# Optimization experiments

Hardware: AMD Instinct MI355X
Metric: run time of the kernel (lower is better)

## Reference

```python
import math
import jax, jax.numpy as jnp
from jax import lax
import numpy as np

B, S2, D = 8, 1024, 768  # seq_len = 32*32 spatial tokens
HD = 64                   # head_dim
K = 7                     # LocalRmsNorm kernel_size
EPS = 1e-7


def setup_inputs() -> dict:
    key = jax.random.key(0)
    ks = jax.random.split(key, 6)
    sc = 0.02
    return {
        "x": jax.random.normal(ks[0], (B, S2, D), jnp.float32),
        "norm_w": jnp.ones((D,), jnp.float32),
        "wq": jax.random.normal(ks[1], (D, D), jnp.float32) * sc,
        "bq": jnp.zeros((D,), jnp.float32),
        "wk": jax.random.normal(ks[2], (D, D), jnp.float32) * sc,
        "bk": jnp.zeros((D,), jnp.float32),
        "wv": jax.random.normal(ks[3], (D, D), jnp.float32) * sc,
        "bv": jnp.zeros((D,), jnp.float32),
        "wo": jax.random.normal(ks[4], (D, D), jnp.float32) * sc,
        "bo": jnp.zeros((D,), jnp.float32),
    }


def local_rms_norm(x, w):
    # x: [b, s*s, d]; sliding KxK box-sum of squares over the s x s grid,
    # zero-padded (matches F.unfold), mean divisor is always K*K.
    b, ss, d = x.shape
    s = int(math.isqrt(ss))
    sq = (x * x).reshape(b, s, s, d)
    box = lax.reduce_window(sq, 0.0, lax.add,
                            (1, K, K, 1), (1, 1, 1, 1), 'SAME')
    rms = jnp.sqrt(EPS + box / (K * K)).reshape(b, ss, d)
    return x / rms * w


def reference(x, norm_w, wq, bq, wk, bk, wv, bv, wo, bo):
    xn = local_rms_norm(x, norm_w)
    b, s, d = xn.shape
    h = d // HD

    def proj(w_, b_):
        return (xn @ w_.T + b_).reshape(b, s, h, HD).transpose(0, 2, 1, 3)

    q = proj(wq, bq)  # [b, h, s, dh]
    k = proj(wk, bk)
    v = proj(wv, bv)
    scores = jnp.einsum('bhqd,bhkd->bhqk', q, k) / math.sqrt(HD)
    attn = jax.nn.softmax(scores, axis=-1)
    out = jnp.einsum('bhqk,bhkd->bhqd', attn, v)
    out = out.transpose(0, 2, 1, 3).reshape(b, s, d)
    return out @ wo.T + bo
```

## Files before the change

### kernel.cpp

```cpp
#include <hip/hip_runtime.h>

typedef _Float16 f16x8 __attribute__((ext_vector_type(8)));
typedef _Float16 f16x4 __attribute__((ext_vector_type(4)));
typedef _Float16 f16x2 __attribute__((ext_vector_type(2)));
typedef float    f32x4 __attribute__((ext_vector_type(4)));
typedef float    f32x16 __attribute__((ext_vector_type(16)));
typedef unsigned int u32x4 __attribute__((ext_vector_type(4)));
typedef unsigned short ushort_t;
typedef unsigned int uint_t;

#define LOG2E 1.44269504088896340736f

#define CFENCE  asm volatile("" ::: "memory")
#define HWBAR   __builtin_amdgcn_s_barrier()
#define VMCNT0  asm volatile("s_waitcnt vmcnt(0)" ::: "memory")
#define VMCNT3  asm volatile("s_waitcnt vmcnt(3)" ::: "memory")
#define VMCNT4  asm volatile("s_waitcnt vmcnt(4)" ::: "memory")

__device__ __forceinline__ ushort_t f2h(float x) {
  _Float16 h = (_Float16)x;
  return __builtin_bit_cast(ushort_t, h);
}

__device__ __forceinline__ uint_t packpair(float a, float b) {
  return __builtin_bit_cast(uint_t, __builtin_amdgcn_cvt_pkrtz(a, b));
}

__device__ __forceinline__ f16x8 mk8(uint_t a, uint_t b, uint_t c, uint_t d) {
  u32x4 t; t[0] = a; t[1] = b; t[2] = c; t[3] = d;
  return __builtin_bit_cast(f16x8, t);
}

__device__ __forceinline__ void gload_lds16(const void* g, void* lds) {
  __builtin_amdgcn_global_load_lds(
      (const __attribute__((address_space(1))) void*)(uintptr_t)g,
      (__attribute__((address_space(3))) void*)(unsigned)(uintptr_t)lds,
      16, 0, 0);
}


__global__ __launch_bounds__(256)
void lrn_a(const float* __restrict__ x, ushort_t* __restrict__ tmp) {
  int tid = blockIdx.x * 256 + threadIdx.x;
  int dv  = tid % 192;
  int rem = tid / 192;
  int pos = rem & 1023;
  int b   = rem >> 10;
  int r = pos >> 5, c = pos & 31;
  const float4* base = (const float4*)x + ((size_t)b * 1024 + (size_t)r * 32) * 192 + dv;
  float ax = 0.f, ay = 0.f, az = 0.f, aw = 0.f;
#pragma unroll
  for (int dc = -3; dc <= 3; ++dc) {
    int cc = c + dc;
    if (cc >= 0 && cc < 32) {
      float4 v = base[cc * 192];
      ax += v.x * v.x; ay += v.y * v.y; az += v.z * v.z; aw += v.w * v.w;
    }
  }
  f16x4 o;
  o[0] = (_Float16)ax; o[1] = (_Float16)ay; o[2] = (_Float16)az; o[3] = (_Float16)aw;
  *(f16x4*)(tmp + (size_t)tid * 4) = o;
}

__global__ __launch_bounds__(256)
void lrn_b(const float* __restrict__ x, const ushort_t* __restrict__ tmp,
           const float* __restrict__ wn, ushort_t* __restrict__ xn) {
  int tid = blockIdx.x * 256 + threadIdx.x;
  int dv  = tid % 192;
  int rem = tid / 192;
  int pos = rem & 1023;
  int b   = rem >> 10;
  int r = pos >> 5, c = pos & 31;
  const ushort_t* tb = tmp + (((size_t)b * 1024 + c) * 192 + dv) * 4;
  float ax = 0.f, ay = 0.f, az = 0.f, aw = 0.f;
#pragma unroll
  for (int dr = -3; dr <= 3; ++dr) {
    int rr = r + dr;
    if (rr >= 0 && rr < 32) {
      f16x4 v = *(const f16x4*)(tb + (size_t)rr * 24576);
      ax += (float)v[0]; ay += (float)v[1]; az += (float)v[2]; aw += (float)v[3];
    }
  }
  float4 xv = ((const float4*)x)[tid];
  float4 wv = ((const float4*)wn)[dv];
  const float inv49 = 1.0f / 49.0f;
  float i0 = 1.0f / sqrtf(1e-7f + ax * inv49);
  float i1 = 1.0f / sqrtf(1e-7f + ay * inv49);
  float i2 = 1.0f / sqrtf(1e-7f + az * inv49);
  float i3 = 1.0f / sqrtf(1e-7f + aw * inv49);
  f16x4 o;
  o[0] = (_Float16)(xv.x * i0 * wv.x);
  o[1] = (_Float16)(xv.y * i1 * wv.y);
  o[2] = (_Float16)(xv.z * i2 * wv.z);
  o[3] = (_Float16)(xv.w * i3 * wv.w);
  const int m = b * 1024 + pos;
  const int panel = m >> 4, lrr = m & 15;
  const int kc = dv >> 3, lg2 = (dv >> 1) & 3, half = dv & 1;
  *(f16x4*)(xn + ((size_t)((panel * 24 + kc) * 64 + lg2 * 16 + lrr)) * 8 + half * 4) = o;
}

__global__ __launch_bounds__(256)
void convw_fm(const float* __restrict__ wq, const float* __restrict__ wk,
              const float* __restrict__ wv, const float* __restrict__ wo,
              ushort_t* __restrict__ bqkv, ushort_t* __restrict__ bwo) {
  const int g = blockIdx.x * 256 + threadIdx.x;
  const int mat = g / 73728;
  const int gg = g % 73728;
  const int panel = gg / 1536;
  const int rem = gg % 1536;
  const int kc = rem >> 6, l = rem & 63;
  const int row = panel * 16 + (l & 15);
  const int col = kc * 32 + (l >> 4) * 8;
  const float* src = (mat == 0) ? wq : (mat == 1) ? wk : (mat == 2) ? wv : wo;
  const float4 v0 = *(const float4*)(src + (size_t)row * 768 + col);
  const float4 v1 = *(const float4*)(src + (size_t)row * 768 + col + 4);
  f16x8 o;
  o[0]=(_Float16)v0.x; o[1]=(_Float16)v0.y; o[2]=(_Float16)v0.z; o[3]=(_Float16)v0.w;
  o[4]=(_Float16)v1.x; o[5]=(_Float16)v1.y; o[6]=(_Float16)v1.z; o[7]=(_Float16)v1.w;
  if (mat < 3) *(f16x8*)(bqkv + (size_t)g * 8) = o;
  else         *(f16x8*)(bwo  + (size_t)gg * 8) = o;
}

#define GSTAGE(BUF, KT) do {                                                      \
    _Pragma("unroll")                                                             \
    for (int j = 0; j < SI; ++j)                                                  \
      gload_lds16(sb[j] + (KT) * 512, (BUF) ? d1[j] : d0[j]);                     \
  } while (0)

#define GTILE(KT, CUR, NXT) do {                                                  \
    CFENCE; HWBAR; CFENCE;                              \
    if ((KT) + 1 < 24) {                                                          \
      GSTAGE(NXT, (KT) + 1);                                                      \
      if constexpr (SI == 4) VMCNT4; else VMCNT3;       \
    } else VMCNT0;                                                                \
    CFENCE; HWBAR;                                \
    __builtin_amdgcn_sched_barrier(0);                                            \
    f16x8 af[MT], bf[NT];                                                         \
    _Pragma("unroll")                                                             \
    for (int mt = 0; mt < MT; ++mt)                                               \
      af[mt] = *(const f16x8*)(&As[CUR][(wr * MT + mt) * 512 + l * 8]);           \
    _Pragma("unroll")                                                             \
    for (int nt = 0; nt < NT; ++nt)                                               \
      bf[nt] = *(const f16x8*)(&Bs[CUR][(wc * NT + nt) * 512 + l * 8]);           \
    _Pragma("unroll")                                                             \
    for (int mt = 0; mt < MT; ++mt)                                               \
      _Pragma("unroll")                                                           \
      for (int nt = 0; nt < NT; ++nt)                                             \
        acc[mt][nt] = __builtin_amdgcn_mfma_f32_16x16x32_f16(af[mt], bf[nt], acc[mt][nt], 0, 0, 0); \
  } while (0)

template <int MODE>
__global__ __launch_bounds__(256)
void gemm_lds(const ushort_t* __restrict__ Afm, const ushort_t* __restrict__ Bfm,
              const float* __restrict__ b0, const float* __restrict__ b1,
              const float* __restrict__ b2,
              ushort_t* __restrict__ q, ushort_t* __restrict__ k,
              ushort_t* __restrict__ v, float* __restrict__ outf) {
  constexpr int PM  = (MODE == 0) ? 8 : 4;
  constexpr int PN  = 8;
  constexpr int NBN = (MODE == 0) ? 18 : 6;
  constexpr int SI  = (PM + PN) / 4;
  constexpr int MT  = PM / 2, NT = PN / 2;
  __shared__ __align__(16) ushort_t As[2][PM * 512];
  __shared__ __align__(16) ushort_t Bs[2][PN * 512];

  const int nwg = gridDim.x;
  const int bid = blockIdx.x;
  const int cid = (bid & 7) * (nwg >> 3) + (bid >> 3);
  const int bm = cid / NBN, bn = cid % NBN;
  const int tid = threadIdx.x;
  const int w = tid >> 6, l = tid & 63;
  const int wr = w >> 1, wc = w & 1;
  const int lr = l & 15, lg = l >> 4;

  f32x4 acc[MT][NT] = {};

  const ushort_t* sb[SI];
  ushort_t* d0[SI];
  ushort_t* d1[SI];
#pragma unroll
  for (int j = 0; j < SI; ++j) {
    const int g = w * SI + j;
    if (g < PM) {
      sb[j] = Afm + ((size_t)(bm * PM + g) * 24) * 512 + l * 8;
      d0[j] = &As[0][g * 512]; d1[j] = &As[1][g * 512];
    } else {
      sb[j] = Bfm + ((size_t)(bn * PN + (g - PM)) * 24) * 512 + l * 8;
      d0[j] = &Bs[0][(g - PM) * 512]; d1[j] = &Bs[1][(g - PM) * 512];
    }
  }

  GSTAGE(0, 0);
  for (int kt = 0; kt < 24; kt += 2) {
    GTILE(kt, 0, 1);
    GTILE(kt + 1, 1, 0);
  }

#pragma unroll
  for (int mt = 0; mt < MT; ++mt) {
#pragma unroll
    for (int nt = 0; nt < NT; ++nt) {
      if (MODE == 0) {
        const int n = bn * 128 + wc * 64 + nt * 16 + lr;
        const int mbase = bm * 128 + wr * 64 + mt * 16 + lg * 4;
        const int region = n / 768;
        const int nn = n - region * 768;
        const int hh = nn >> 6, hd = nn & 63;
        const float bb = (region == 0 ? b0 : region == 1 ? b1 : b2)[nn];
        if (region == 2) {
          const int bi = mbase >> 10, s0 = mbase & 1023;
          const int tile = s0 >> 6, q6 = s0 & 63;
          const int aa = q6 >> 5, r5 = q6 & 31;
          const int t1 = r5 >> 3, h2 = (r5 >> 2) & 1;
          const int gq = t1 >> 1, jj = (2 * t1) & 3;
          const int s0p = (tile << 6) + (((aa << 1) + gq) << 4) + (h2 << 3) + 2 * jj;
          f16x4 pv;
#pragma unroll
          for (int gi = 0; gi < 4; ++gi) pv[gi] = (_Float16)(acc[mt][nt][gi] + bb);
          *(f16x4*)(v + (((size_t)(bi * 12 + hh)) * 64 + hd) * 1024 + s0p) = pv;
        } else {
#pragma unroll
          for (int gi = 0; gi < 4; ++gi) {
            const int m = mbase + gi;
            const int bi = m >> 10, s = m & 1023;
            const float val = acc[mt][nt][gi] + bb;
            if (region == 0)
              q[(((size_t)(bi * 12 + hh)) * 1024 + s) * 64 + hd] = f2h(val * (0.125f * LOG2E));
            else
              k[(((size_t)(bi * 12 + hh)) * 1024 + s) * 64 + hd] = f2h(val);
          }
        }
      } else {
        const int n = bn * 128 + wc * 64 + nt * 16 + lr;
        const float bb = b0[n];
#pragma unroll
        for (int gi = 0; gi < 4; ++gi) {
          const int m = bm * 64 + wr * 32 + mt * 16 + lg * 4 + gi;
          outf[(size_t)m * 768 + n] = acc[mt][nt][gi] + bb;
        }
      }
    }
  }
}

#define ATILE(T, CUR, NXT) do {                                                   \
    CFENCE; HWBAR; CFENCE;                              \
    if ((T) < 15) {                                                               \
      const int kv0n = ((T) + 1) << 6;                                            \
      gload_lds16(kp + (size_t)(kv0n + r1) * 64 + s1 * 8,  Kl0 + (NXT) * 8192);   \
      gload_lds16(kp + (size_t)(kv0n + r2) * 64 + s2 * 8,  Kl1 + (NXT) * 8192);   \
      gload_lds16(vp + (size_t)r1 * 1024 + kv0n + s1 * 8,  Vl0 + (NXT) * 8192);   \
      gload_lds16(vp + (size_t)r2 * 1024 + kv0n + s2 * 8,  Vl1 + (NXT) * 8192);   \
      VMCNT4;                                        \
    } else VMCNT0;                                                                \
    CFENCE; HWBAR;                            \
    __builtin_amdgcn_sched_barrier(0);                                            \
    const char* kbase = (const char*)smem + (CUR) * 8192;                         \
    const char* vbase = (const char*)smem + 16384 + (CUR) * 8192;                 \
    f16x8 ka0[4], ka1[4];                                                         \
    _Pragma("unroll")                                                             \
    for (int kc = 0; kc < 4; ++kc) {                                              \
      ka0[kc] = *(const f16x8*)(kbase + off[kc]);                                 \
      ka1[kc] = *(const f16x8*)(kbase + off[kc] + 4096);                          \
    }                                                                             \
    f32x16 s0v = {}, s1v = {};                                                    \
    __builtin_amdgcn_s_setprio(1);                                                \
    _Pragma("unroll")                                                             \
    for (int kc = 0; kc < 4; ++kc) {                                              \
      s0v = __builtin_amdgcn_mfma_f32_32x32x16_f16(ka0[kc], qf[kc], s0v, 0, 0, 0);\
      s1v = __builtin_amdgcn_mfma_f32_32x32x16_f16(ka1[kc], qf[kc], s1v, 0, 0, 0);\
    }                                                                             \
    __builtin_amdgcn_s_setprio(0);                                                \
    f16x8 va0[4], va1[4];                                                         \
    _Pragma("unroll")                                                             \
    for (int c = 0; c < 4; ++c) {                                                 \
      va0[c] = *(const f16x8*)(vbase + off[c]);                                   \
      va1[c] = *(const f16x8*)(vbase + off[c] + 4096);                            \
    }                                                                             \
    uint_t pk0[8], pk1[8];                                                        \
    _Pragma("unroll")                                                             \
    for (int tt = 0; tt < 8; ++tt) {                                              \
      pk0[tt] = packpair(__builtin_exp2f(s0v[2 * tt]), __builtin_exp2f(s0v[2 * tt + 1])); \
      pk1[tt] = packpair(__builtin_exp2f(s1v[2 * tt]), __builtin_exp2f(s1v[2 * tt + 1])); \
    }                                                                             \
    _Pragma("unroll")                                                             \
    for (int tt = 0; tt < 4; ++tt) {                                              \
      lr0 = __builtin_amdgcn_fdot2(__builtin_bit_cast(f16x2, pk0[tt]),     one2, lr0, false); \
      lr1 = __builtin_amdgcn_fdot2(__builtin_bit_cast(f16x2, pk0[tt + 4]), one2, lr1, false); \
      lr2 = __builtin_amdgcn_fdot2(__builtin_bit_cast(f16x2, pk1[tt]),     one2, lr2, false); \
      lr3 = __builtin_amdgcn_fdot2(__builtin_bit_cast(f16x2, pk1[tt + 4]), one2, lr3, false); \
    }                                                                             \
    const f16x8 pb0 = mk8(pk0[0], pk0[1], pk0[2], pk0[3]);                        \
    const f16x8 pb1 = mk8(pk0[4], pk0[5], pk0[6], pk0[7]);                        \
    const f16x8 pb2 = mk8(pk1[0], pk1[1], pk1[2], pk1[3]);                        \
    const f16x8 pb3 = mk8(pk1[4], pk1[5], pk1[6], pk1[7]);                        \
    __builtin_amdgcn_s_setprio(1);                                                \
    oacc0 = __builtin_amdgcn_mfma_f32_32x32x16_f16(va0[0], pb0, oacc0, 0, 0, 0);  \
    oacc1 = __builtin_amdgcn_mfma_f32_32x32x16_f16(va1[0], pb0, oacc1, 0, 0, 0);  \
    oacc0 = __builtin_amdgcn_mfma_f32_32x32x16_f16(va0[1], pb1, oacc0, 0, 0, 0);  \
    oacc1 = __builtin_amdgcn_mfma_f32_32x32x16_f16(va1[1], pb1, oacc1, 0, 0, 0);  \
    oacc0 = __builtin_amdgcn_mfma_f32_32x32x16_f16(va0[2], pb2, oacc0, 0, 0, 0);  \
    oacc1 = __builtin_amdgcn_mfma_f32_32x32x16_f16(va1[2], pb2, oacc1, 0, 0, 0);  \
    oacc0 = __builtin_amdgcn_mfma_f32_32x32x16_f16(va0[3], pb3, oacc0, 0, 0, 0);  \
    oacc1 = __builtin_amdgcn_mfma_f32_32x32x16_f16(va1[3], pb3, oacc1, 0, 0, 0);  \
    __builtin_amdgcn_s_setprio(0);                                                \
  } while (0)

__global__ __launch_bounds__(256, 3)
void attn_fused7(const ushort_t* __restrict__ qb, const ushort_t* __restrict__ kb,
                 const ushort_t* __restrict__ vt, ushort_t* __restrict__ ao) {
  __shared__ __align__(16) ushort_t smem[16384];
  const int tid = threadIdx.x;
  const int w = tid >> 6, l = tid & 63;
  const int lq = l & 31, hi = l >> 5;

  const int bid = blockIdx.x;
  const int cid = (bid & 7) * 96 + (bid >> 3);
  const int bh = cid >> 3, qt = cid & 7;
  const int b = bh / 12, h = bh % 12;

  const ushort_t* qp = qb + ((size_t)bh * 1024 + qt * 128 + w * 32) * 64;
  const ushort_t* kp = kb + (size_t)bh * 65536;
  const ushort_t* vp = vt + (size_t)bh * 65536;

  f16x8 qf[4];
#pragma unroll
  for (int kc = 0; kc < 4; ++kc)
    qf[kc] = *(const f16x8*)(qp + lq * 64 + kc * 16 + hi * 8);

  const int r1 = tid >> 3,          s1 = (tid & 7) ^ (r1 & 7);
  const int r2 = (tid + 256) >> 3,  s2 = (tid & 7) ^ (r2 & 7);
  char* Kl0 = (char*)smem + w * 1024;
  char* Kl1 = (char*)smem + 4096 + w * 1024;
  char* Vl0 = (char*)smem + 16384 + w * 1024;
  char* Vl1 = (char*)smem + 16384 + 4096 + w * 1024;

  const int cswz = lq & 7;
  int off[4];
#pragma unroll
  for (int kc = 0; kc < 4; ++kc)
    off[kc] = lq * 128 + (((kc * 2 + hi) ^ cswz) * 16);

  f32x16 oacc0 = {}, oacc1 = {};
  float lr0 = 0.f, lr1 = 0.f, lr2 = 0.f, lr3 = 0.f;
  const f16x2 one2 = {(_Float16)1.f, (_Float16)1.f};

  gload_lds16(kp + (size_t)r1 * 64 + s1 * 8,   Kl0);
  gload_lds16(kp + (size_t)r2 * 64 + s2 * 8,   Kl1);
  gload_lds16(vp + (size_t)r1 * 1024 + s1 * 8, Vl0);
  gload_lds16(vp + (size_t)r2 * 1024 + s2 * 8, Vl1);

  for (int t2 = 0; t2 < 16; t2 += 2) {
    ATILE(t2, 0, 1);
    ATILE(t2 + 1, 1, 0);
  }

  float lrun = (lr0 + lr1) + (lr2 + lr3);
  lrun += __shfl_xor(lrun, 32, 64);
  const float invl = 1.0f / lrun;

  __syncthreads();

  uint_t* ot = (uint_t*)smem + w * 1024 + lq * 32;
#pragma unroll
  for (int tt = 0; tt < 8; ++tt) {
    const int base = (tt & 1) + ((tt >> 1) << 2) + 2 * hi;
    ot[base ^ lq]        = packpair(oacc0[2 * tt] * invl, oacc0[2 * tt + 1] * invl);
    ot[(base + 16) ^ lq] = packpair(oacc1[2 * tt] * invl, oacc1[2 * tt + 1] * invl);
  }
  __syncthreads();
  const int row = tid >> 1, halfc = tid & 1;
  const int w2 = row >> 5, qq = row & 31;
  const uint_t* srcp = (const uint_t*)smem + w2 * 1024 + qq * 32;
  const int m = b * 1024 + qt * 128 + row;
  const int panel = m >> 4, lrr = m & 15;
  const int kc = h * 2 + halfc;
#pragma unroll
  for (int jj = 0; jj < 4; ++jj) {
    u32x4 tv;
#pragma unroll
    for (int i2 = 0; i2 < 4; ++i2)
      tv[i2] = srcp[(halfc * 16 + jj * 4 + i2) ^ qq];
    *(u32x4*)(ao + ((size_t)((panel * 24 + kc) * 64 + jj * 16 + lrr)) * 8) = tv;
  }
}

extern "C" void kernel_launch(void* const* d_in, const int* in_sizes, int n_in,
                              void* d_out, int out_size, void* d_ws, size_t ws_size,
                              hipStream_t stream) {
  const float* x  = (const float*)d_in[0];
  const float* nw = (const float*)d_in[1];
  const float* wq = (const float*)d_in[2];
  const float* bq = (const float*)d_in[3];
  const float* wk = (const float*)d_in[4];
  const float* bk = (const float*)d_in[5];
  const float* wv = (const float*)d_in[6];
  const float* bv = (const float*)d_in[7];
  const float* wo = (const float*)d_in[8];
  const float* bo = (const float*)d_in[9];
  float* out = (float*)d_out;

  char* ws = (char*)d_ws;
  ushort_t* tmp   = (ushort_t*)ws;
  ushort_t* qbuf  = (ushort_t*)(ws);
  ushort_t* kbuf  = (ushort_t*)(ws + 12582912);
  ushort_t* xnf   = (ushort_t*)(ws + 25165824);
  ushort_t* bwqkv = (ushort_t*)(ws + 37748736);
  ushort_t* bwo   = (ushort_t*)(ws + 41287680);
  ushort_t* vtb   = (ushort_t*)(ws + 42467328);
  ushort_t* aoutf = (ushort_t*)(ws + 55050240);

  lrn_a<<<6144, 256, 0, stream>>>(x, tmp);
  lrn_b<<<6144, 256, 0, stream>>>(x, tmp, nw, xnf);
  convw_fm<<<1152, 256, 0, stream>>>(wq, wk, wv, wo, bwqkv, bwo);
  gemm_lds<0><<<1152, 256, 0, stream>>>(xnf, bwqkv, bq, bk, bv,
                                        qbuf, kbuf, vtb, nullptr);
  attn_fused7<<<768, 256, 0, stream>>>(qbuf, kbuf, vtb, aoutf);
  gemm_lds<1><<<768, 256, 0, stream>>>(aoutf, bwo, bo, nullptr, nullptr,
                                       nullptr, nullptr, nullptr, out);
}
```

Baseline: 147.3 us.

## Triple-buffer LDS tiles in attention and output GEMM to drop a barrier

The attention kernel and the output-projection GEMM move from double- to triple-buffered LDS staging with a rotating buffer index. Because the buffer being refilled was last read two iterations earlier, the barrier that used to come before issuing the next prefetch is removed, leaving one workgroup barrier per tile. The aim is to cut synchronisation stalls and let global-to-LDS loads overlap compute further. In exchange, attention LDS per block grows from 32KB to 48KB, which may limit occupancy at 3 blocks per CU, and the templated GEMM is split into two specialised kernels.

```diff
diff --git a/kernel.cpp b/kernel.cpp
--- a/kernel.cpp
+++ b/kernel.cpp
@@ -131,7 +131,7 @@
     CFENCE; HWBAR; CFENCE;                              \
     if ((KT) + 1 < 24) {                                                          \
       GSTAGE(NXT, (KT) + 1);                                                      \
-      if constexpr (SI == 4) VMCNT4; else VMCNT3;       \
+      VMCNT4;                                           \
     } else VMCNT0;                                                                \
     CFENCE; HWBAR;                                \
     __builtin_amdgcn_sched_barrier(0);                                            \
@@ -149,18 +149,13 @@
         acc[mt][nt] = __builtin_amdgcn_mfma_f32_16x16x32_f16(af[mt], bf[nt], acc[mt][nt], 0, 0, 0); \
   } while (0)
 
-template <int MODE>
 __global__ __launch_bounds__(256)
-void gemm_lds(const ushort_t* __restrict__ Afm, const ushort_t* __restrict__ Bfm,
+void gemm_qkv(const ushort_t* __restrict__ Afm, const ushort_t* __restrict__ Bfm,
               const float* __restrict__ b0, const float* __restrict__ b1,
               const float* __restrict__ b2,
               ushort_t* __restrict__ q, ushort_t* __restrict__ k,
-              ushort_t* __restrict__ v, float* __restrict__ outf) {
-  constexpr int PM  = (MODE == 0) ? 8 : 4;
-  constexpr int PN  = 8;
-  constexpr int NBN = (MODE == 0) ? 18 : 6;
-  constexpr int SI  = (PM + PN) / 4;
-  constexpr int MT  = PM / 2, NT = PN / 2;
+              ushort_t* __restrict__ v) {
+  constexpr int PM = 8, PN = 8, NBN = 18, SI = 4, MT = 4, NT = 4;
   __shared__ __align__(16) ushort_t As[2][PM * 512];
   __shared__ __align__(16) ushort_t Bs[2][PN * 512];
 
@@ -200,116 +195,113 @@
   for (int mt = 0; mt < MT; ++mt) {
 #pragma unroll
     for (int nt = 0; nt < NT; ++nt) {
-      if (MODE == 0) {
-        const int n = bn * 128 + wc * 64 + nt * 16 + lr;
-        const int mbase = bm * 128 + wr * 64 + mt * 16 + lg * 4;
-        const int region = n / 768;
-        const int nn = n - region * 768;
-        const int hh = nn >> 6, hd = nn & 63;
-        const float bb = (region == 0 ? b0 : region == 1 ? b1 : b2)[nn];
-        if (region == 2) {
-          const int bi = mbase >> 10, s0 = mbase & 1023;
-          const int tile = s0 >> 6, q6 = s0 & 63;
-          const int aa = q6 >> 5, r5 = q6 & 31;
-          const int t1 = r5 >> 3, h2 = (r5 >> 2) & 1;
-          const int gq = t1 >> 1, jj = (2 * t1) & 3;
-          const int s0p = (tile << 6) + (((aa << 1) + gq) << 4) + (h2 << 3) + 2 * jj;
-          f16x4 pv;
-#pragma unroll
-          for (int gi = 0; gi < 4; ++gi) pv[gi] = (_Float16)(acc[mt][nt][gi] + bb);
-          *(f16x4*)(v + (((size_t)(bi * 12 + hh)) * 64 + hd) * 1024 + s0p) = pv;
-        } else {
-#pragma unroll
-          for (int gi = 0; gi < 4; ++gi) {
-            const int m = mbase + gi;
-            const int bi = m >> 10, s = m & 1023;
-            const float val = acc[mt][nt][gi] + bb;
-            if (region == 0)
-              q[(((size_t)(bi * 12 + hh)) * 1024 + s) * 64 + hd] = f2h(val * (0.125f * LOG2E));
-            else
-              k[(((size_t)(bi * 12 + hh)) * 1024 + s) * 64 + hd] = f2h(val);
-          }
-        }
+      const int n = bn * 128 + wc * 64 + nt * 16 + lr;
+      const int mbase = bm * 128 + wr * 64 + mt * 16 + lg * 4;
+      const int region = n / 768;
+      const int nn = n - region * 768;
+      const int hh = nn >> 6, hd = nn & 63;
+      const float bb = (region == 0 ? b0 : region == 1 ? b1 : b2)[nn];
+      if (region == 2) {
+        const int bi = mbase >> 10, s0 = mbase & 1023;
+        const int tile = s0 >> 6, q6 = s0 & 63;
+        const int aa = q6 >> 5, r5 = q6 & 31;
+        const int t1 = r5 >> 3, h2 = (r5 >> 2) & 1;
+        const int gq = t1 >> 1, jj = (2 * t1) & 3;
+        const int s0p = (tile << 6) + (((aa << 1) + gq) << 4) + (h2 << 3) + 2 * jj;
+        f16x4 pv;
+#pragma unroll
+        for (int gi = 0; gi < 4; ++gi) pv[gi] = (_Float16)(acc[mt][nt][gi] + bb);
+        *(f16x4*)(v + (((size_t)(bi * 12 + hh)) * 64 + hd) * 1024 + s0p) = pv;
       } else {
-        const int n = bn * 128 + wc * 64 + nt * 16 + lr;
-        const float bb = b0[n];
 #pragma unroll
         for (int gi = 0; gi < 4; ++gi) {
-          const int m = bm * 64 + wr * 32 + mt * 16 + lg * 4 + gi;
-          outf[(size_t)m * 768 + n] = acc[mt][nt][gi] + bb;
+          const int m = mbase + gi;
+          const int bi = m >> 10, s = m & 1023;
+          const float val = acc[mt][nt][gi] + bb;
+          if (region == 0)
+            q[(((size_t)(bi * 12 + hh)) * 1024 + s) * 64 + hd] = f2h(val * (0.125f * LOG2E));
+          else
+            k[(((size_t)(bi * 12 + hh)) * 1024 + s) * 64 + hd] = f2h(val);
         }
       }
     }
   }
 }
 
-#define ATILE(T, CUR, NXT) do {                                                   \
-    CFENCE; HWBAR; CFENCE;                              \
-    if ((T) < 15) {                                                               \
-      const int kv0n = ((T) + 1) << 6;                                            \
-      gload_lds16(kp + (size_t)(kv0n + r1) * 64 + s1 * 8,  Kl0 + (NXT) * 8192);   \
-      gload_lds16(kp + (size_t)(kv0n + r2) * 64 + s2 * 8,  Kl1 + (NXT) * 8192);   \
-      gload_lds16(vp + (size_t)r1 * 1024 + kv0n + s1 * 8,  Vl0 + (NXT) * 8192);   \
-      gload_lds16(vp + (size_t)r2 * 1024 + kv0n + s2 * 8,  Vl1 + (NXT) * 8192);   \
-      VMCNT4;                                        \
-    } else VMCNT0;                                                                \
-    CFENCE; HWBAR;                            \
-    __builtin_amdgcn_sched_barrier(0);                                            \
-    const char* kbase = (const char*)smem + (CUR) * 8192;                         \
-    const char* vbase = (const char*)smem + 16384 + (CUR) * 8192;                 \
-    f16x8 ka0[4], ka1[4];                                                         \
-    _Pragma("unroll")                                                             \
-    for (int kc = 0; kc < 4; ++kc) {                                              \
-      ka0[kc] = *(const f16x8*)(kbase + off[kc]);                                 \
-      ka1[kc] = *(const f16x8*)(kbase + off[kc] + 4096);                          \
-    }                                                                             \
-    f32x16 s0v = {}, s1v = {};                                                    \
-    __builtin_amdgcn_s_setprio(1);                                                \
-    _Pragma("unroll")                                                             \
-    for (int kc = 0; kc < 4; ++kc) {                                              \
-      s0v = __builtin_amdgcn_mfma_f32_32x32x16_f16(ka0[kc], qf[kc], s0v, 0, 0, 0);\
-      s1v = __builtin_amdgcn_mfma_f32_32x32x16_f16(ka1[kc], qf[kc], s1v, 0, 0, 0);\
-    }                                                                             \
-    __builtin_amdgcn_s_setprio(0);                                                \
-    f16x8 va0[4], va1[4];                                                         \
-    _Pragma("unroll")                                                             \
-    for (int c = 0; c < 4; ++c) {                                                 \
-      va0[c] = *(const f16x8*)(vbase + off[c]);                                   \
-      va1[c] = *(const f16x8*)(vbase + off[c] + 4096);                            \
-    }                                                                             \
-    uint_t pk0[8], pk1[8];                                                        \
-    _Pragma("unroll")                                                             \
-    for (int tt = 0; tt < 8; ++tt) {                                              \
-      pk0[tt] = packpair(__builtin_exp2f(s0v[2 * tt]), __builtin_exp2f(s0v[2 * tt + 1])); \
-      pk1[tt] = packpair(__builtin_exp2f(s1v[2 * tt]), __builtin_exp2f(s1v[2 * tt + 1])); \
-    }                                                                             \
-    _Pragma("unroll")                                                             \
-    for (int tt = 0; tt < 4; ++tt) {                                              \
-      lr0 = __builtin_amdgcn_fdot2(__builtin_bit_cast(f16x2, pk0[tt]),     one2, lr0, false); \
-      lr1 = __builtin_amdgcn_fdot2(__builtin_bit_cast(f16x2, pk0[tt + 4]), one2, lr1, false); \
-      lr2 = __builtin_amdgcn_fdot2(__builtin_bit_cast(f16x2, pk1[tt]),     one2, lr2, false); \
-      lr3 = __builtin_amdgcn_fdot2(__builtin_bit_cast(f16x2, pk1[tt + 4]), one2, lr3, false); \
-    }                                                                             \
-    const f16x8 pb0 = mk8(pk0[0], pk0[1], pk0[2], pk0[3]);                        \
-    const f16x8 pb1 = mk8(pk0[4], pk0[5], pk0[6], pk0[7]);                        \
-    const f16x8 pb2 = mk8(pk1[0], pk1[1], pk1[2], pk1[3]);                        \
-    const f16x8 pb3 = mk8(pk1[4], pk1[5], pk1[6], pk1[7]);                        \
-    __builtin_amdgcn_s_setprio(1);                                                \
-    oacc0 = __builtin_amdgcn_mfma_f32_32x32x16_f16(va0[0], pb0, oacc0, 0, 0, 0);  \
-    oacc1 = __builtin_amdgcn_mfma_f32_32x32x16_f16(va1[0], pb0, oacc1, 0, 0, 0);  \
-    oacc0 = __builtin_amdgcn_mfma_f32_32x32x16_f16(va0[1], pb1, oacc0, 0, 0, 0);  \
-    oacc1 = __builtin_amdgcn_mfma_f32_32x32x16_f16(va1[1], pb1, oacc1, 0, 0, 0);  \
-    oacc0 = __builtin_amdgcn_mfma_f32_32x32x16_f16(va0[2], pb2, oacc0, 0, 0, 0);  \
-    oacc1 = __builtin_amdgcn_mfma_f32_32x32x16_f16(va1[2], pb2, oacc1, 0, 0, 0);  \
-    oacc0 = __builtin_amdgcn_mfma_f32_32x32x16_f16(va0[3], pb3, oacc0, 0, 0, 0);  \
-    oacc1 = __builtin_amdgcn_mfma_f32_32x32x16_f16(va1[3], pb3, oacc1, 0, 0, 0);  \
-    __builtin_amdgcn_s_setprio(0);                                                \
-  } while (0)
+__global__ __launch_bounds__(256)
+void gemm_wo(const ushort_t* __restrict__ Afm, const ushort_t* __restrict__ Bfm,
+             const float* __restrict__ b0, float* __restrict__ outf) {
+  __shared__ __align__(16) ushort_t Asf[3 * 4 * 512];
+  __shared__ __align__(16) ushort_t Bsf[3 * 8 * 512];
+
+  const int bid = blockIdx.x;
+  const int cid = (bid & 7) * 96 + (bid >> 3);
+  const int bm = cid / 6, bn = cid % 6;
+  const int tid = threadIdx.x;
+  const int w = tid >> 6, l = tid & 63;
+  const int wr = w >> 1, wc = w & 1;
+  const int lr = l & 15, lg = l >> 4;
+
+  f32x4 acc[2][4] = {};
+
+  const ushort_t* sb[3];
+  ushort_t* dA[3];
+  bool isA[3];
+#pragma unroll
+  for (int j = 0; j < 3; ++j) {
+    const int g = w * 3 + j;
+    isA[j] = (g < 4);
+    if (g < 4) { sb[j] = Afm + ((size_t)(bm * 4 + g) * 24) * 512 + l * 8;        dA[j] = &Asf[g * 512]; }
+    else       { sb[j] = Bfm + ((size_t)(bn * 8 + (g - 4)) * 24) * 512 + l * 8;  dA[j] = &Bsf[(g - 4) * 512]; }
+  }
+
+#pragma unroll
+  for (int j = 0; j < 3; ++j) gload_lds16(sb[j], dA[j]);
+
+  int cur = 0;
+  for (int kt = 0; kt < 24; ++kt) {
+    if (kt < 23) {
+      const int nxt = (cur == 2) ? 0 : cur + 1;
+#pragma unroll
+      for (int j = 0; j < 3; ++j)
+        gload_lds16(sb[j] + (kt + 1) * 512, dA[j] + (isA[j] ? nxt * 2048 : nxt * 4096));
+      VMCNT3;
+    } else VMCNT0;
+    CFENCE; HWBAR;
+    __builtin_amdgcn_sched_barrier(0);
+    f16x8 af[2], bf[4];
+#pragma unroll
+    for (int mt = 0; mt < 2; ++mt)
+      af[mt] = *(const f16x8*)(&Asf[cur * 2048 + (wr * 2 + mt) * 512 + l * 8]);
+#pragma unroll
+    for (int nt = 0; nt < 4; ++nt)
+      bf[nt] = *(const f16x8*)(&Bsf[cur * 4096 + (wc * 4 + nt) * 512 + l * 8]);
+#pragma unroll
+    for (int mt = 0; mt < 2; ++mt)
+#pragma unroll
+      for (int nt = 0; nt < 4; ++nt)
+        acc[mt][nt] = __builtin_amdgcn_mfma_f32_16x16x32_f16(af[mt], bf[nt], acc[mt][nt], 0, 0, 0);
+    cur = (cur == 2) ? 0 : cur + 1;
+  }
+
+#pragma unroll
+  for (int mt = 0; mt < 2; ++mt)
+#pragma unroll
+    for (int nt = 0; nt < 4; ++nt) {
+      const int n = bn * 128 + wc * 64 + nt * 16 + lr;
+      const float bb = b0[n];
+#pragma unroll
+      for (int gi = 0; gi < 4; ++gi) {
+        const int m = bm * 64 + wr * 32 + mt * 16 + lg * 4 + gi;
+        outf[(size_t)m * 768 + n] = acc[mt][nt][gi] + bb;
+      }
+    }
+}
 
 __global__ __launch_bounds__(256, 3)
-void attn_fused7(const ushort_t* __restrict__ qb, const ushort_t* __restrict__ kb,
+void attn_fused8(const ushort_t* __restrict__ qb, const ushort_t* __restrict__ kb,
                  const ushort_t* __restrict__ vt, ushort_t* __restrict__ ao) {
-  __shared__ __align__(16) ushort_t smem[16384];
+  __shared__ __align__(16) ushort_t smem[24576];
   const int tid = threadIdx.x;
   const int w = tid >> 6, l = tid & 63;
   const int lq = l & 31, hi = l >> 5;
@@ -332,8 +324,8 @@
   const int r2 = (tid + 256) >> 3,  s2 = (tid & 7) ^ (r2 & 7);
   char* Kl0 = (char*)smem + w * 1024;
   char* Kl1 = (char*)smem + 4096 + w * 1024;
-  char* Vl0 = (char*)smem + 16384 + w * 1024;
-  char* Vl1 = (char*)smem + 16384 + 4096 + w * 1024;
+  char* Vl0 = (char*)smem + 24576 + w * 1024;
+  char* Vl1 = (char*)smem + 24576 + 4096 + w * 1024;
 
   const int cswz = lq & 7;
   int off[4];
@@ -350,9 +342,76 @@
   gload_lds16(vp + (size_t)r1 * 1024 + s1 * 8, Vl0);
   gload_lds16(vp + (size_t)r2 * 1024 + s2 * 8, Vl1);
 
-  for (int t2 = 0; t2 < 16; t2 += 2) {
-    ATILE(t2, 0, 1);
-    ATILE(t2 + 1, 1, 0);
+  int cur = 0;
+  for (int t = 0; t < 16; ++t) {
+    if (t < 15) {
+      const int nxt = (cur == 2) ? 0 : cur + 1;
+      const int no = nxt * 8192;
+      const int kv0n = (t + 1) << 6;
+      gload_lds16(kp + (size_t)(kv0n + r1) * 64 + s1 * 8,  Kl0 + no);
+      gload_lds16(kp + (size_t)(kv0n + r2) * 64 + s2 * 8,  Kl1 + no);
+      gload_lds16(vp + (size_t)r1 * 1024 + kv0n + s1 * 8,  Vl0 + no);
+      gload_lds16(vp + (size_t)r2 * 1024 + kv0n + s2 * 8,  Vl1 + no);
+      VMCNT4;
+    } else VMCNT0;
+    CFENCE; HWBAR;
+    __builtin_amdgcn_sched_barrier(0);
+
+    const char* kbase = (const char*)smem + cur * 8192;
+    const char* vbase = (const char*)smem + 24576 + cur * 8192;
+
+    f16x8 ka0[4], ka1[4];
+#pragma unroll
+    for (int kc = 0; kc < 4; ++kc) {
+      ka0[kc] = *(const f16x8*)(kbase + off[kc]);
+      ka1[kc] = *(const f16x8*)(kbase + off[kc] + 4096);
+    }
+    f32x16 s0v = {}, s1v = {};
+    __builtin_amdgcn_s_setprio(1);
+#pragma unroll
+    for (int kc = 0; kc < 4; ++kc) {
+      s0v = __builtin_amdgcn_mfma_f32_32x32x16_f16(ka0[kc], qf[kc], s0v, 0, 0, 0);
+      s1v = __builtin_amdgcn_mfma_f32_32x32x16_f16(ka1[kc], qf[kc], s1v, 0, 0, 0);
+    }
+    __builtin_amdgcn_s_setprio(0);
+
+    f16x8 va0[4], va1[4];
+#pragma unroll
+    for (int c = 0; c < 4; ++c) {
+      va0[c] = *(const f16x8*)(vbase + off[c]);
+      va1[c] = *(const f16x8*)(vbase + off[c] + 4096);
+    }
+
+    uint_t pk0[8], pk1[8];
+#pragma unroll
+    for (int tt = 0; tt < 8; ++tt) {
+      pk0[tt] = packpair(__builtin_exp2f(s0v[2 * tt]), __builtin_exp2f(s0v[2 * tt + 1]));
+      pk1[tt] = packpair(__builtin_exp2f(s1v[2 * tt]), __builtin_exp2f(s1v[2 * tt + 1]));
+    }
+#pragma unroll
+    for (int tt = 0; tt < 4; ++tt) {
+      lr0 = __builtin_amdgcn_fdot2(__builtin_bit_cast(f16x2, pk0[tt]),     one2, lr0, false);
+      lr1 = __builtin_amdgcn_fdot2(__builtin_bit_cast(f16x2, pk0[tt + 4]), one2, lr1, false);
+      lr2 = __builtin_amdgcn_fdot2(__builtin_bit_cast(f16x2, pk1[tt]),     one2, lr2, false);
+      lr3 = __builtin_amdgcn_fdot2(__builtin_bit_cast(f16x2, pk1[tt + 4]), one2, lr3, false);
+    }
+    const f16x8 pb0 = mk8(pk0[0], pk0[1], pk0[2], pk0[3]);
+    const f16x8 pb1 = mk8(pk0[4], pk0[5], pk0[6], pk0[7]);
+    const f16x8 pb2 = mk8(pk1[0], pk1[1], pk1[2], pk1[3]);
+    const f16x8 pb3 = mk8(pk1[4], pk1[5], pk1[6], pk1[7]);
+
+    __builtin_amdgcn_s_setprio(1);
+    oacc0 = __builtin_amdgcn_mfma_f32_32x32x16_f16(va0[0], pb0, oacc0, 0, 0, 0);
+    oacc1 = __builtin_amdgcn_mfma_f32_32x32x16_f16(va1[0], pb0, oacc1, 0, 0, 0);
+    oacc0 = __builtin_amdgcn_mfma_f32_32x32x16_f16(va0[1], pb1, oacc0, 0, 0, 0);
+    oacc1 = __builtin_amdgcn_mfma_f32_32x32x16_f16(va1[1], pb1, oacc1, 0, 0, 0);
+    oacc0 = __builtin_amdgcn_mfma_f32_32x32x16_f16(va0[2], pb2, oacc0, 0, 0, 0);
+    oacc1 = __builtin_amdgcn_mfma_f32_32x32x16_f16(va1[2], pb2, oacc1, 0, 0, 0);
+    oacc0 = __builtin_amdgcn_mfma_f32_32x32x16_f16(va0[3], pb3, oacc0, 0, 0, 0);
+    oacc1 = __builtin_amdgcn_mfma_f32_32x32x16_f16(va1[3], pb3, oacc1, 0, 0, 0);
+    __builtin_amdgcn_s_setprio(0);
+
+    cur = (cur == 2) ? 0 : cur + 1;
   }
 
   float lrun = (lr0 + lr1) + (lr2 + lr3);
@@ -413,9 +472,7 @@
   lrn_a<<<6144, 256, 0, stream>>>(x, tmp);
   lrn_b<<<6144, 256, 0, stream>>>(x, tmp, nw, xnf);
   convw_fm<<<1152, 256, 0, stream>>>(wq, wk, wv, wo, bwqkv, bwo);
-  gemm_lds<0><<<1152, 256, 0, stream>>>(xnf, bwqkv, bq, bk, bv,
-                                        qbuf, kbuf, vtb, nullptr);
-  attn_fused7<<<768, 256, 0, stream>>>(qbuf, kbuf, vtb, aoutf);
-  gemm_lds<1><<<768, 256, 0, stream>>>(aoutf, bwo, bo, nullptr, nullptr,
-                                       nullptr, nullptr, nullptr, out);
-}
+  gemm_qkv<<<1152, 256, 0, stream>>>(xnf, bwqkv, bq, bk, bv, qbuf, kbuf, vtb);
+  attn_fused8<<<768, 256, 0, stream>>>(qbuf, kbuf, vtb, aoutf);
+  gemm_wo<<<768, 256, 0, stream>>>(aoutf, bwo, bo, out);
+}
```

Result: no change. 147.5 us (+0.1%).
